# Performance work log

Measured on AMD Instinct MI355X. Metric: run time of the kernel, lower is better.

The kernel has to match this reference:

```python
import jax, jax.numpy as jnp
import numpy as np
import math

N, CH, T, S = 32, 64, 2048, 77  # batch*heads, per-head channels, query len, encoder len

def setup_inputs() -> dict:
    key = jax.random.key(0)
    k1, k2 = jax.random.split(key)
    qkv = jax.random.normal(k1, (N, 3 * CH, T), dtype=jnp.float32)
    encoder_kv = jax.random.normal(k2, (N, 2 * CH, S), dtype=jnp.float32)
    attn_mask = jnp.zeros((1, T, S + T), dtype=jnp.float32)
    return {"qkv": qkv, "encoder_kv": encoder_kv, "attn_mask": attn_mask}

def reference(qkv, encoder_kv, attn_mask):
    ch = qkv.shape[1] // 3
    q, k, v = jnp.split(qkv, 3, axis=1)          # each [N, ch, T]
    ek, ev = jnp.split(encoder_kv, 2, axis=1)    # each [N, ch, S]
    k = jnp.concatenate([ek, k], axis=-1)        # [N, ch, S+T]
    v = jnp.concatenate([ev, v], axis=-1)
    scale = 1.0 / math.sqrt(math.sqrt(ch))
    weight = jnp.einsum('bct,bcs->bts', q * scale, k * scale)  # [N, T, S+T]
    weight = weight.astype(jnp.float32) + attn_mask
    weight = jax.nn.softmax(weight, axis=-1).astype(v.dtype)
    return jnp.einsum('bts,bcs->bct', weight, v)  # [N, ch, T]
```

## Files before the change

kernel.cpp:

```cpp
#include <hip/hip_runtime.h>


typedef __attribute__((ext_vector_type(8))) __bf16 bf16x8;
typedef __attribute__((ext_vector_type(8))) unsigned short u16x8;
typedef __attribute__((ext_vector_type(4))) float f32x4;
typedef float f32x4a __attribute__((ext_vector_type(4))) __attribute__((aligned(4)));
typedef __attribute__((ext_vector_type(4))) unsigned u32x4;
typedef __attribute__((ext_vector_type(2))) unsigned u32x2;

#define L2E  1.44269504089f
#define NEGM (-23.0830936f)

static __device__ __forceinline__ unsigned short f2bf(float f) {
    unsigned u = __builtin_bit_cast(unsigned, f);
    u += 0x7fffu + ((u >> 16) & 1u);
    return (unsigned short)(u >> 16);
}

static __device__ __forceinline__ unsigned pack_bf16(float a, float b) {
#if __has_builtin(__builtin_amdgcn_cvt_pk_bf16_f32)
    typedef __bf16 bf16x2_t __attribute__((ext_vector_type(2)));
    bf16x2_t r = __builtin_amdgcn_cvt_pk_bf16_f32(a, b);
    unsigned u; __builtin_memcpy(&u, &r, 4);
    return u;
#else
    unsigned ua = __builtin_bit_cast(unsigned, a);
    unsigned ub = __builtin_bit_cast(unsigned, b);
    ua += 0x7fffu + ((ua >> 16) & 1u);
    ub += 0x7fffu + ((ub >> 16) & 1u);
    return __builtin_amdgcn_perm(ub, ua, 0x07060302u);
#endif
}

__global__ __launch_bounds__(256) void prep_all(const float* __restrict__ qkv,
                                                const float* __restrict__ ekv,
                                                unsigned short* __restrict__ kws,
                                                unsigned short* __restrict__ vws,
                                                const float* __restrict__ mask) {
    int b = blockIdx.x;
    int tid = threadIdx.x;

    if (b >= 3136) {
        int bb = b - 3136;
        const u32x4* m4 = (const u32x4*)mask;
        unsigned acc = 0;
        for (int i = (bb << 8) + tid; i < 1088000; i += 131072) {
            u32x4 x = m4[i];
            acc |= x.x | x.y | x.z | x.w;
        }
        if (acc) atomicOr((unsigned*)(kws + (size_t)2175 * 64), 1u);
        return;
    }

    if (b >= 1088) {
        int bb = b - 1088;
        int n = bb >> 6, c = bb & 63;
        const float* v  = qkv + (size_t)n * 192 * 2048 + (size_t)(128 + c) * 2048;
        const float* ev = ekv + (size_t)n * 128 * 77 + (size_t)(64 + c) * 77;
        unsigned short* dst = vws + ((size_t)n * 64 + c) * 2176;
        for (int u = tid; u < 544; u += 256) {
            int s = u << 2;
            float f[4];
            if (u >= 20 && u <= 530) {
                f32x4a x = *(const f32x4a*)(v + s - 77);
                f[0] = x.x; f[1] = x.y; f[2] = x.z; f[3] = x.w;
            } else {
                #pragma unroll
                for (int k = 0; k < 4; ++k) {
                    int sk = s + k;
                    f[k] = (sk < 77) ? ev[sk] : ((sk < 2125) ? v[sk - 77] : 0.f);
                }
            }
            u32x2 pk; pk.x = pack_bf16(f[0], f[1]); pk.y = pack_bf16(f[2], f[3]);
            *(u32x2*)(dst + s) = pk;
        }
        return;
    }

    __shared__ float tile[64][65];
    int mode, n, t0;
    if (b < 1024) { mode = 1; n = b >> 5;          t0 = (b & 31) << 6; }
    else          { mode = 2; n = (b - 1024) >> 1; t0 = ((b - 1024) & 1) << 6; }

    const float* src;
    size_t srow;
    int tmax = 64;
    if (mode == 1) { src = qkv + (size_t)n * 192 * 2048 + (size_t)64 * 2048 + t0; srow = 2048; }
    else           { src = ekv + (size_t)n * 128 * 77 + t0; srow = 77;
                     tmax = 77 - t0; if (tmax > 64) tmax = 64; }

    #pragma unroll
    for (int i = 0; i < 4; ++i) {
        int idx = tid + (i << 8);
        int c  = idx >> 4;
        int t4 = (idx & 15) << 2;
        const float* p = src + (size_t)c * srow + t4;
        float v0, v1, v2, v3;
        if (mode == 1) {
            f32x4 v = *(const f32x4*)p;
            v0 = v.x; v1 = v.y; v2 = v.z; v3 = v.w;
        } else {
            v0 = (t4 + 0 < tmax) ? p[0] : 0.f;
            v1 = (t4 + 1 < tmax) ? p[1] : 0.f;
            v2 = (t4 + 2 < tmax) ? p[2] : 0.f;
            v3 = (t4 + 3 < tmax) ? p[3] : 0.f;
        }
        tile[t4 + 0][c] = v0;
        tile[t4 + 1][c] = v1;
        tile[t4 + 2][c] = v2;
        tile[t4 + 3][c] = v3;
    }
    __syncthreads();
    #pragma unroll
    for (int i = 0; i < 4; ++i) {
        int idx = tid + (i << 8);
        int row = idx >> 4;
        int c4  = (idx & 15) << 2;
        if (mode == 2 && row >= tmax) continue;
        u32x2 pk;
        pk.x = pack_bf16(tile[row][c4 + 0], tile[row][c4 + 1]);
        pk.y = pack_bf16(tile[row][c4 + 2], tile[row][c4 + 3]);
        unsigned short* dst;
        if (mode == 1) dst = kws + ((size_t)n * 2176 + 77 + t0 + row) * 64;
        else           dst = kws + ((size_t)n * 2176 + t0 + row) * 64;
        *(u32x2*)(dst + c4) = pk;
    }
}

__global__ __launch_bounds__(256, 2) void flash_attn(
        const float* __restrict__ qkv,
        const unsigned short* __restrict__ kws,
        const unsigned short* __restrict__ vws,
        const float* __restrict__ mask,
        float* __restrict__ out) {
    __shared__ alignas(16) unsigned short k_lds[2][64 * 72];
    __shared__ alignas(16) unsigned short v_lds[3][64 * 72];
    __shared__ alignas(16) unsigned short p_lds[4][32 * 72];

    const int n    = blockIdx.y;
    const int t0   = blockIdx.x << 7;
    const int tid  = threadIdx.x;
    const int wave = tid >> 6;
    const int lane = tid & 63;
    const int q    = lane >> 4;
    const int l16  = lane & 15;
    const int tc0  = t0 + (wave << 5) + l16;
    const int tc1  = tc0 + 16;

    const bool domask =
        __builtin_amdgcn_readfirstlane(*(const unsigned*)(kws + (size_t)2175 * 64)) != 0u;

    bf16x8 qf[2][2];
    #pragma unroll
    for (int h = 0; h < 2; ++h) {
        const float* qsrc = qkv + (size_t)n * 192 * 2048 + (h ? tc1 : tc0);
        u16x8 a0, a1;
        #pragma unroll
        for (int j = 0; j < 8; ++j) {
            a0[j] = f2bf(qsrc[(size_t)((q << 3) + j) * 2048] * 0.125f);
            a1[j] = f2bf(qsrc[(size_t)(32 + (q << 3) + j) * 2048] * 0.125f);
        }
        qf[h][0] = __builtin_bit_cast(bf16x8, a0);
        qf[h][1] = __builtin_bit_cast(bf16x8, a1);
    }

    const unsigned short* kg = kws + (size_t)n * 2176 * 64;
    const unsigned short* vg = vws + (size_t)n * 64 * 2176;
    const float* mrow0 = mask + (size_t)tc0 * 2125;
    const float* mrow1 = mask + (size_t)tc1 * 2125;
    unsigned short* const pw0 = p_lds[wave] + (size_t)l16 * 72;
    unsigned short* const pw1 = p_lds[wave] + (size_t)(16 + l16) * 72;

    const int srow0 = tid >> 3,        sch = (tid & 7) << 3;
    const int srow1 = srow0 + 32;

    f32x4 of[2][4] = {};
    f32x4 sacc[4][2];
    float lsum0 = 0.f, lsum1 = 0.f;

    u32x4 kreg[2], vreg[2];
    f32x4 mreg[4][2];

    auto issue_kv = [&](int s0) {
        kreg[0] = *(const u32x4*)(kg + (size_t)(s0 + srow0) * 64 + sch);
        vreg[0] = *(const u32x4*)(vg + (size_t)srow0 * 2176 + s0 + sch);
        kreg[1] = *(const u32x4*)(kg + (size_t)(s0 + srow1) * 64 + sch);
        vreg[1] = *(const u32x4*)(vg + (size_t)srow1 * 2176 + s0 + sch);
    };
    auto issue_mask = [&](int s0) {
        #pragma unroll
        for (int sm = 0; sm < 4; ++sm) {
            int sbase = s0 + (sm << 4) + (q << 2);
            int sclamp = sbase > 2121 ? 2121 : sbase;
            f32x4a m0 = *(const f32x4a*)(mrow0 + sclamp);
            f32x4a m1 = *(const f32x4a*)(mrow1 + sclamp);
            mreg[sm][0] = f32x4{m0.x, m0.y, m0.z, m0.w};
            mreg[sm][1] = f32x4{m1.x, m1.y, m1.z, m1.w};
        }
    };
    auto stage = [&](unsigned short* kb, unsigned short* vb) {
        *(u32x4*)(kb + srow0 * 72 + sch) = kreg[0];
        *(u32x4*)(vb + srow0 * 72 + sch) = vreg[0];
        *(u32x4*)(kb + srow1 * 72 + sch) = kreg[1];
        *(u32x4*)(vb + srow1 * 72 + sch) = vreg[1];
    };
    auto qkm = [&](const unsigned short* kb) {
        #pragma unroll
        for (int sm = 0; sm < 4; ++sm) {
            const unsigned short* kp = kb + (size_t)((sm << 4) + l16) * 72 + (q << 3);
            bf16x8 ak0 = *(const bf16x8*)(kp);
            bf16x8 ak1 = *(const bf16x8*)(kp + 32);
            #pragma unroll
            for (int h = 0; h < 2; ++h) {
                f32x4 a = {};
                a = __builtin_amdgcn_mfma_f32_16x16x32_bf16(ak0, qf[h][0], a, 0, 0, 0);
                a = __builtin_amdgcn_mfma_f32_16x16x32_bf16(ak1, qf[h][1], a, 0, 0, 0);
                sacc[sm][h] = a;
            }
        }
    };
    auto smax = [&](int s0) {
        const bool tail = (s0 + 64 > 2125);
        #pragma unroll
        for (int sm = 0; sm < 4; ++sm) {
            int sbase = s0 + (sm << 4) + (q << 2);
            #pragma unroll
            for (int h = 0; h < 2; ++h) {
                f32x4 a = sacc[sm][h];
                if (domask) a += mreg[sm][h];
                if (tail) {
                    #pragma unroll
                    for (int j = 0; j < 4; ++j)
                        if (sbase + j >= 2125) a[j] = -1e30f;
                }
                float p0 = __builtin_amdgcn_exp2f(__builtin_fmaf(a[0], L2E, NEGM));
                float p1 = __builtin_amdgcn_exp2f(__builtin_fmaf(a[1], L2E, NEGM));
                float p2 = __builtin_amdgcn_exp2f(__builtin_fmaf(a[2], L2E, NEGM));
                float p3 = __builtin_amdgcn_exp2f(__builtin_fmaf(a[3], L2E, NEGM));
                if (h) lsum1 += (p0 + p1) + (p2 + p3);
                else   lsum0 += (p0 + p1) + (p2 + p3);
                u32x2 pk; pk.x = pack_bf16(p0, p1); pk.y = pack_bf16(p2, p3);
                *(u32x2*)((h ? pw1 : pw0) + (sm << 4) + (q << 2)) = pk;
            }
        }
    };
    auto pv = [&](const unsigned short* vb) {
        bf16x8 bp00 = *(const bf16x8*)(pw0 + (q << 3));
        bf16x8 bp01 = *(const bf16x8*)(pw0 + (q << 3) + 32);
        bf16x8 bp10 = *(const bf16x8*)(pw1 + (q << 3));
        bf16x8 bp11 = *(const bf16x8*)(pw1 + (q << 3) + 32);
        #pragma unroll
        for (int cm = 0; cm < 4; ++cm) {
            const unsigned short* vp = vb + (size_t)((cm << 4) + l16) * 72 + (q << 3);
            bf16x8 av0 = *(const bf16x8*)(vp);
            bf16x8 av1 = *(const bf16x8*)(vp + 32);
            of[0][cm] = __builtin_amdgcn_mfma_f32_16x16x32_bf16(av0, bp00, of[0][cm], 0, 0, 0);
            of[0][cm] = __builtin_amdgcn_mfma_f32_16x16x32_bf16(av1, bp01, of[0][cm], 0, 0, 0);
            of[1][cm] = __builtin_amdgcn_mfma_f32_16x16x32_bf16(av0, bp10, of[1][cm], 0, 0, 0);
            of[1][cm] = __builtin_amdgcn_mfma_f32_16x16x32_bf16(av1, bp11, of[1][cm], 0, 0, 0);
        }
    };

    issue_kv(0);
    if (domask) issue_mask(0);
    stage(k_lds[0], v_lds[0]);
    __syncthreads();
    issue_kv(64);
    qkm(k_lds[0]);
    smax(0);
    if (domask) issue_mask(64);

    int vri = 0, vwi = 1;
    for (int ks = 0; ks < 33; ++ks) {
        const int s1 = (ks + 1) << 6;
        stage(k_lds[(ks + 1) & 1], v_lds[vwi]);
        __syncthreads();
        if (ks < 32) issue_kv(s1 + 64);
        qkm(k_lds[(ks + 1) & 1]);
        pv(v_lds[vri]);
        smax(s1);
        if (domask && ks < 32) issue_mask(s1 + 64);
        vri = (vri == 2) ? 0 : vri + 1;
        vwi = (vwi == 2) ? 0 : vwi + 1;
    }
    pv(v_lds[vri]);

    lsum0 += __shfl_xor(lsum0, 16, 64);
    lsum0 += __shfl_xor(lsum0, 32, 64);
    lsum1 += __shfl_xor(lsum1, 16, 64);
    lsum1 += __shfl_xor(lsum1, 32, 64);
    float inv0 = 1.0f / lsum0, inv1 = 1.0f / lsum1;
    #pragma unroll
    for (int cm = 0; cm < 4; ++cm)
        #pragma unroll
        for (int j = 0; j < 4; ++j) {
            int c = (cm << 4) + (q << 2) + j;
            float* o = out + ((size_t)n * 64 + c) * 2048;
            o[tc0] = of[0][cm][j] * inv0;
            o[tc1] = of[1][cm][j] * inv1;
        }
}

extern "C" void kernel_launch(void* const* d_in, const int* in_sizes, int n_in,
                              void* d_out, int out_size, void* d_ws, size_t ws_size,
                              hipStream_t stream) {
    const float* qkv  = (const float*)d_in[0];
    const float* ekv  = (const float*)d_in[1];
    const float* mask = (const float*)d_in[2];
    float* out = (float*)d_out;

    unsigned short* kws = (unsigned short*)d_ws;
    unsigned short* vws = kws + (size_t)32 * 2176 * 64;

    hipMemsetAsync((char*)d_ws + (size_t)2175 * 64 * 2, 0, 4, stream);
    prep_all<<<3648, 256, 0, stream>>>(qkv, ekv, kws, vws, mask);
    dim3 grid(16, 32);
    flash_attn<<<grid, 256, 0, stream>>>(qkv, kws, vws, mask, out);
}
```

Measured before the change: 163.0 us.

## Halve query tile per wave, load V fragments directly from global

```diff
diff --git a/kernel.cpp b/kernel.cpp
--- a/kernel.cpp
+++ b/kernel.cpp
@@ -127,82 +127,70 @@
     }
 }
 
-__global__ __launch_bounds__(256, 2) void flash_attn(
+__global__ __launch_bounds__(256, 4) void flash_attn(
         const float* __restrict__ qkv,
         const unsigned short* __restrict__ kws,
         const unsigned short* __restrict__ vws,
         const float* __restrict__ mask,
         float* __restrict__ out) {
     __shared__ alignas(16) unsigned short k_lds[2][64 * 72];
-    __shared__ alignas(16) unsigned short v_lds[3][64 * 72];
-    __shared__ alignas(16) unsigned short p_lds[4][32 * 72];
+    __shared__ alignas(16) unsigned short p_lds[4][16 * 72];
 
     const int n    = blockIdx.y;
-    const int t0   = blockIdx.x << 7;
+    const int t0   = blockIdx.x << 6;
     const int tid  = threadIdx.x;
     const int wave = tid >> 6;
     const int lane = tid & 63;
     const int q    = lane >> 4;
     const int l16  = lane & 15;
-    const int tc0  = t0 + (wave << 5) + l16;
-    const int tc1  = tc0 + 16;
+    const int tc   = t0 + (wave << 4) + l16;
 
     const bool domask =
         __builtin_amdgcn_readfirstlane(*(const unsigned*)(kws + (size_t)2175 * 64)) != 0u;
 
-    bf16x8 qf[2][2];
-    #pragma unroll
-    for (int h = 0; h < 2; ++h) {
-        const float* qsrc = qkv + (size_t)n * 192 * 2048 + (h ? tc1 : tc0);
+    bf16x8 qf[2];
+    {
+        const float* qsrc = qkv + (size_t)n * 192 * 2048 + tc;
         u16x8 a0, a1;
         #pragma unroll
         for (int j = 0; j < 8; ++j) {
             a0[j] = f2bf(qsrc[(size_t)((q << 3) + j) * 2048] * 0.125f);
             a1[j] = f2bf(qsrc[(size_t)(32 + (q << 3) + j) * 2048] * 0.125f);
         }
-        qf[h][0] = __builtin_bit_cast(bf16x8, a0);
-        qf[h][1] = __builtin_bit_cast(bf16x8, a1);
+        qf[0] = __builtin_bit_cast(bf16x8, a0);
+        qf[1] = __builtin_bit_cast(bf16x8, a1);
     }
 
     const unsigned short* kg = kws + (size_t)n * 2176 * 64;
     const unsigned short* vg = vws + (size_t)n * 64 * 2176;
-    const float* mrow0 = mask + (size_t)tc0 * 2125;
-    const float* mrow1 = mask + (size_t)tc1 * 2125;
-    unsigned short* const pw0 = p_lds[wave] + (size_t)l16 * 72;
-    unsigned short* const pw1 = p_lds[wave] + (size_t)(16 + l16) * 72;
-
-    const int srow0 = tid >> 3,        sch = (tid & 7) << 3;
+    const float* mrow = mask + (size_t)tc * 2125;
+    unsigned short* const pw = p_lds[wave] + (size_t)l16 * 72;
+
+    const int srow0 = tid >> 3, sch = (tid & 7) << 3;
     const int srow1 = srow0 + 32;
 
-    f32x4 of[2][4] = {};
-    f32x4 sacc[4][2];
-    float lsum0 = 0.f, lsum1 = 0.f;
-
-    u32x4 kreg[2], vreg[2];
-    f32x4 mreg[4][2];
-
-    auto issue_kv = [&](int s0) {
+    f32x4 of[4] = {};
+    f32x4 sacc[4];
+    float lsum = 0.f;
+
+    u32x4 kreg[2];
+    bf16x8 vfrag[4][2];
+
+    auto issue_k = [&](int s0) {
         kreg[0] = *(const u32x4*)(kg + (size_t)(s0 + srow0) * 64 + sch);
-        vreg[0] = *(const u32x4*)(vg + (size_t)srow0 * 2176 + s0 + sch);
         kreg[1] = *(const u32x4*)(kg + (size_t)(s0 + srow1) * 64 + sch);
-        vreg[1] = *(const u32x4*)(vg + (size_t)srow1 * 2176 + s0 + sch);
-    };
-    auto issue_mask = [&](int s0) {
-        #pragma unroll
-        for (int sm = 0; sm < 4; ++sm) {
-            int sbase = s0 + (sm << 4) + (q << 2);
-            int sclamp = sbase > 2121 ? 2121 : sbase;
-            f32x4a m0 = *(const f32x4a*)(mrow0 + sclamp);
-            f32x4a m1 = *(const f32x4a*)(mrow1 + sclamp);
-            mreg[sm][0] = f32x4{m0.x, m0.y, m0.z, m0.w};
-            mreg[sm][1] = f32x4{m1.x, m1.y, m1.z, m1.w};
-        }
-    };
-    auto stage = [&](unsigned short* kb, unsigned short* vb) {
+    };
+    auto issue_v = [&](int s0) {
+        #pragma unroll
+        for (int cm = 0; cm < 4; ++cm) {
+            const unsigned short* vp = vg + (size_t)((cm << 4) + l16) * 2176 + s0 + (q << 3);
+            vfrag[cm][0] = *(const bf16x8*)(vp);
+            vfrag[cm][1] = *(const bf16x8*)(vp + 32);
+        }
+    };
+    auto stage = [&](unsigned short* kb) {
         *(u32x4*)(kb + srow0 * 72 + sch) = kreg[0];
-        *(u32x4*)(vb + srow0 * 72 + sch) = vreg[0];
         *(u32x4*)(kb + srow1 * 72 + sch) = kreg[1];
-        *(u32x4*)(vb + srow1 * 72 + sch) = vreg[1];
     };
     auto qkm = [&](const unsigned short* kb) {
         #pragma unroll
@@ -210,13 +198,10 @@
             const unsigned short* kp = kb + (size_t)((sm << 4) + l16) * 72 + (q << 3);
             bf16x8 ak0 = *(const bf16x8*)(kp);
             bf16x8 ak1 = *(const bf16x8*)(kp + 32);
-            #pragma unroll
-            for (int h = 0; h < 2; ++h) {
-                f32x4 a = {};
-                a = __builtin_amdgcn_mfma_f32_16x16x32_bf16(ak0, qf[h][0], a, 0, 0, 0);
-                a = __builtin_amdgcn_mfma_f32_16x16x32_bf16(ak1, qf[h][1], a, 0, 0, 0);
-                sacc[sm][h] = a;
-            }
+            f32x4 a = {};
+            a = __builtin_amdgcn_mfma_f32_16x16x32_bf16(ak0, qf[0], a, 0, 0, 0);
+            a = __builtin_amdgcn_mfma_f32_16x16x32_bf16(ak1, qf[1], a, 0, 0, 0);
+            sacc[sm] = a;
         }
     };
     auto smax = [&](int s0) {
@@ -224,80 +209,65 @@
         #pragma unroll
         for (int sm = 0; sm < 4; ++sm) {
             int sbase = s0 + (sm << 4) + (q << 2);
-            #pragma unroll
-            for (int h = 0; h < 2; ++h) {
-                f32x4 a = sacc[sm][h];
-                if (domask) a += mreg[sm][h];
-                if (tail) {
-                    #pragma unroll
-                    for (int j = 0; j < 4; ++j)
-                        if (sbase + j >= 2125) a[j] = -1e30f;
-                }
-                float p0 = __builtin_amdgcn_exp2f(__builtin_fmaf(a[0], L2E, NEGM));
-                float p1 = __builtin_amdgcn_exp2f(__builtin_fmaf(a[1], L2E, NEGM));
-                float p2 = __builtin_amdgcn_exp2f(__builtin_fmaf(a[2], L2E, NEGM));
-                float p3 = __builtin_amdgcn_exp2f(__builtin_fmaf(a[3], L2E, NEGM));
-                if (h) lsum1 += (p0 + p1) + (p2 + p3);
-                else   lsum0 += (p0 + p1) + (p2 + p3);
-                u32x2 pk; pk.x = pack_bf16(p0, p1); pk.y = pack_bf16(p2, p3);
-                *(u32x2*)((h ? pw1 : pw0) + (sm << 4) + (q << 2)) = pk;
+            f32x4 a = sacc[sm];
+            if (domask) {
+                int sclamp = sbase > 2121 ? 2121 : sbase;
+                f32x4a m = *(const f32x4a*)(mrow + sclamp);
+                a[0] += m.x; a[1] += m.y; a[2] += m.z; a[3] += m.w;
             }
-        }
-    };
-    auto pv = [&](const unsigned short* vb) {
-        bf16x8 bp00 = *(const bf16x8*)(pw0 + (q << 3));
-        bf16x8 bp01 = *(const bf16x8*)(pw0 + (q << 3) + 32);
-        bf16x8 bp10 = *(const bf16x8*)(pw1 + (q << 3));
-        bf16x8 bp11 = *(const bf16x8*)(pw1 + (q << 3) + 32);
+            if (tail) {
+                #pragma unroll
+                for (int j = 0; j < 4; ++j)
+                    if (sbase + j >= 2125) a[j] = -1e30f;
+            }
+            float p0 = __builtin_amdgcn_exp2f(__builtin_fmaf(a[0], L2E, NEGM));
+            float p1 = __builtin_amdgcn_exp2f(__builtin_fmaf(a[1], L2E, NEGM));
+            float p2 = __builtin_amdgcn_exp2f(__builtin_fmaf(a[2], L2E, NEGM));
+            float p3 = __builtin_amdgcn_exp2f(__builtin_fmaf(a[3], L2E, NEGM));
+            lsum += (p0 + p1) + (p2 + p3);
+            u32x2 pk; pk.x = pack_bf16(p0, p1); pk.y = pack_bf16(p2, p3);
+            *(u32x2*)(pw + (sm << 4) + (q << 2)) = pk;
+        }
+    };
+    auto pv = [&]() {
+        bf16x8 bp0 = *(const bf16x8*)(pw + (q << 3));
+        bf16x8 bp1 = *(const bf16x8*)(pw + (q << 3) + 32);
         #pragma unroll
         for (int cm = 0; cm < 4; ++cm) {
-            const unsigned short* vp = vb + (size_t)((cm << 4) + l16) * 72 + (q << 3);
-            bf16x8 av0 = *(const bf16x8*)(vp);
-            bf16x8 av1 = *(const bf16x8*)(vp + 32);
-            of[0][cm] = __builtin_amdgcn_mfma_f32_16x16x32_bf16(av0, bp00, of[0][cm], 0, 0, 0);
-            of[0][cm] = __builtin_amdgcn_mfma_f32_16x16x32_bf16(av1, bp01, of[0][cm], 0, 0, 0);
-            of[1][cm] = __builtin_amdgcn_mfma_f32_16x16x32_bf16(av0, bp10, of[1][cm], 0, 0, 0);
-            of[1][cm] = __builtin_amdgcn_mfma_f32_16x16x32_bf16(av1, bp11, of[1][cm], 0, 0, 0);
-        }
-    };
-
-    issue_kv(0);
-    if (domask) issue_mask(0);
-    stage(k_lds[0], v_lds[0]);
+            of[cm] = __builtin_amdgcn_mfma_f32_16x16x32_bf16(vfrag[cm][0], bp0, of[cm], 0, 0, 0);
+            of[cm] = __builtin_amdgcn_mfma_f32_16x16x32_bf16(vfrag[cm][1], bp1, of[cm], 0, 0, 0);
+        }
+    };
+
+    issue_k(0);
+    stage(k_lds[0]);
     __syncthreads();
-    issue_kv(64);
+    issue_k(64);
+    issue_v(0);
     qkm(k_lds[0]);
     smax(0);
-    if (domask) issue_mask(64);
-
-    int vri = 0, vwi = 1;
+
     for (int ks = 0; ks < 33; ++ks) {
         const int s1 = (ks + 1) << 6;
-        stage(k_lds[(ks + 1) & 1], v_lds[vwi]);
+        stage(k_lds[(ks + 1) & 1]);
         __syncthreads();
-        if (ks < 32) issue_kv(s1 + 64);
+        if (ks < 32) issue_k(s1 + 64);
         qkm(k_lds[(ks + 1) & 1]);
-        pv(v_lds[vri]);
+        pv();
+        issue_v(s1);
         smax(s1);
-        if (domask && ks < 32) issue_mask(s1 + 64);
-        vri = (vri == 2) ? 0 : vri + 1;
-        vwi = (vwi == 2) ? 0 : vwi + 1;
-    }
-    pv(v_lds[vri]);
-
-    lsum0 += __shfl_xor(lsum0, 16, 64);
-    lsum0 += __shfl_xor(lsum0, 32, 64);
-    lsum1 += __shfl_xor(lsum1, 16, 64);
-    lsum1 += __shfl_xor(lsum1, 32, 64);
-    float inv0 = 1.0f / lsum0, inv1 = 1.0f / lsum1;
+    }
+    pv();
+
+    lsum += __shfl_xor(lsum, 16, 64);
+    lsum += __shfl_xor(lsum, 32, 64);
+    float inv = 1.0f / lsum;
     #pragma unroll
     for (int cm = 0; cm < 4; ++cm)
         #pragma unroll
         for (int j = 0; j < 4; ++j) {
             int c = (cm << 4) + (q << 2) + j;
-            float* o = out + ((size_t)n * 64 + c) * 2048;
-            o[tc0] = of[0][cm][j] * inv0;
-            o[tc1] = of[1][cm][j] * inv1;
+            out[((size_t)n * 64 + c) * 2048 + tc] = of[cm][j] * inv;
         }
 }
 
@@ -314,6 +284,6 @@
 
     hipMemsetAsync((char*)d_ws + (size_t)2175 * 64 * 2, 0, 4, stream);
     prep_all<<<3648, 256, 0, stream>>>(qkv, ekv, kws, vws, mask);
-    dim3 grid(16, 32);
+    dim3 grid(32, 32);
     flash_attn<<<grid, 256, 0, stream>>>(qkv, kws, vws, mask, out);
 }
```

New measurement: 235.0 us. 1.44x slower.

## Compute softmax row sums via MFMA with ones and drop mask prefetch registers

Applied to the files above, without the earlier changes.

```diff
diff --git a/kernel.cpp b/kernel.cpp
--- a/kernel.cpp
+++ b/kernel.cpp
@@ -164,8 +164,14 @@
         qf[h][1] = __builtin_bit_cast(bf16x8, a1);
     }
 
-    const unsigned short* kg = kws + (size_t)n * 2176 * 64;
-    const unsigned short* vg = vws + (size_t)n * 64 * 2176;
+    bf16x8 ones;
+    {
+        u16x8 o;
+        #pragma unroll
+        for (int j = 0; j < 8; ++j) o[j] = 0x3F80;
+        ones = __builtin_bit_cast(bf16x8, o);
+    }
+
     const float* mrow0 = mask + (size_t)tc0 * 2125;
     const float* mrow1 = mask + (size_t)tc1 * 2125;
     unsigned short* const pw0 = p_lds[wave] + (size_t)l16 * 72;
@@ -174,29 +180,23 @@
     const int srow0 = tid >> 3,        sch = (tid & 7) << 3;
     const int srow1 = srow0 + 32;
 
+    const unsigned short* kp0 = kws + (size_t)n * 2176 * 64 + (size_t)srow0 * 64 + sch;
+    const unsigned short* kp1 = kws + (size_t)n * 2176 * 64 + (size_t)srow1 * 64 + sch;
+    const unsigned short* vp0 = vws + (size_t)n * 64 * 2176 + (size_t)srow0 * 2176 + sch;
+    const unsigned short* vp1 = vws + (size_t)n * 64 * 2176 + (size_t)srow1 * 2176 + sch;
+
     f32x4 of[2][4] = {};
+    f32x4 lacc0 = {}, lacc1 = {};
     f32x4 sacc[4][2];
-    float lsum0 = 0.f, lsum1 = 0.f;
 
     u32x4 kreg[2], vreg[2];
-    f32x4 mreg[4][2];
-
-    auto issue_kv = [&](int s0) {
-        kreg[0] = *(const u32x4*)(kg + (size_t)(s0 + srow0) * 64 + sch);
-        vreg[0] = *(const u32x4*)(vg + (size_t)srow0 * 2176 + s0 + sch);
-        kreg[1] = *(const u32x4*)(kg + (size_t)(s0 + srow1) * 64 + sch);
-        vreg[1] = *(const u32x4*)(vg + (size_t)srow1 * 2176 + s0 + sch);
-    };
-    auto issue_mask = [&](int s0) {
-        #pragma unroll
-        for (int sm = 0; sm < 4; ++sm) {
-            int sbase = s0 + (sm << 4) + (q << 2);
-            int sclamp = sbase > 2121 ? 2121 : sbase;
-            f32x4a m0 = *(const f32x4a*)(mrow0 + sclamp);
-            f32x4a m1 = *(const f32x4a*)(mrow1 + sclamp);
-            mreg[sm][0] = f32x4{m0.x, m0.y, m0.z, m0.w};
-            mreg[sm][1] = f32x4{m1.x, m1.y, m1.z, m1.w};
-        }
+
+    auto issue_kv = [&]() {
+        kreg[0] = *(const u32x4*)kp0;
+        vreg[0] = *(const u32x4*)vp0;
+        kreg[1] = *(const u32x4*)kp1;
+        vreg[1] = *(const u32x4*)vp1;
+        kp0 += 4096; kp1 += 4096; vp0 += 64; vp1 += 64;
     };
     auto stage = [&](unsigned short* kb, unsigned short* vb) {
         *(u32x4*)(kb + srow0 * 72 + sch) = kreg[0];
@@ -227,7 +227,11 @@
             #pragma unroll
             for (int h = 0; h < 2; ++h) {
                 f32x4 a = sacc[sm][h];
-                if (domask) a += mreg[sm][h];
+                if (domask) {
+                    int sclamp = sbase > 2121 ? 2121 : sbase;
+                    f32x4a m = *(const f32x4a*)((h ? mrow1 : mrow0) + sclamp);
+                    a[0] += m.x; a[1] += m.y; a[2] += m.z; a[3] += m.w;
+                }
                 if (tail) {
                     #pragma unroll
                     for (int j = 0; j < 4; ++j)
@@ -237,8 +241,6 @@
                 float p1 = __builtin_amdgcn_exp2f(__builtin_fmaf(a[1], L2E, NEGM));
                 float p2 = __builtin_amdgcn_exp2f(__builtin_fmaf(a[2], L2E, NEGM));
                 float p3 = __builtin_amdgcn_exp2f(__builtin_fmaf(a[3], L2E, NEGM));
-                if (h) lsum1 += (p0 + p1) + (p2 + p3);
-                else   lsum0 += (p0 + p1) + (p2 + p3);
                 u32x2 pk; pk.x = pack_bf16(p0, p1); pk.y = pack_bf16(p2, p3);
                 *(u32x2*)((h ? pw1 : pw0) + (sm << 4) + (q << 2)) = pk;
             }
@@ -249,6 +251,10 @@
         bf16x8 bp01 = *(const bf16x8*)(pw0 + (q << 3) + 32);
         bf16x8 bp10 = *(const bf16x8*)(pw1 + (q << 3));
         bf16x8 bp11 = *(const bf16x8*)(pw1 + (q << 3) + 32);
+        lacc0 = __builtin_amdgcn_mfma_f32_16x16x32_bf16(ones, bp00, lacc0, 0, 0, 0);
+        lacc0 = __builtin_amdgcn_mfma_f32_16x16x32_bf16(ones, bp01, lacc0, 0, 0, 0);
+        lacc1 = __builtin_amdgcn_mfma_f32_16x16x32_bf16(ones, bp10, lacc1, 0, 0, 0);
+        lacc1 = __builtin_amdgcn_mfma_f32_16x16x32_bf16(ones, bp11, lacc1, 0, 0, 0);
         #pragma unroll
         for (int cm = 0; cm < 4; ++cm) {
             const unsigned short* vp = vb + (size_t)((cm << 4) + l16) * 72 + (q << 3);
@@ -261,35 +267,28 @@
         }
     };
 
-    issue_kv(0);
-    if (domask) issue_mask(0);
+    issue_kv();
     stage(k_lds[0], v_lds[0]);
     __syncthreads();
-    issue_kv(64);
+    issue_kv();
     qkm(k_lds[0]);
     smax(0);
-    if (domask) issue_mask(64);
 
     int vri = 0, vwi = 1;
     for (int ks = 0; ks < 33; ++ks) {
         const int s1 = (ks + 1) << 6;
         stage(k_lds[(ks + 1) & 1], v_lds[vwi]);
         __syncthreads();
-        if (ks < 32) issue_kv(s1 + 64);
+        if (ks < 32) issue_kv();
         qkm(k_lds[(ks + 1) & 1]);
         pv(v_lds[vri]);
         smax(s1);
-        if (domask && ks < 32) issue_mask(s1 + 64);
         vri = (vri == 2) ? 0 : vri + 1;
         vwi = (vwi == 2) ? 0 : vwi + 1;
     }
     pv(v_lds[vri]);
 
-    lsum0 += __shfl_xor(lsum0, 16, 64);
-    lsum0 += __shfl_xor(lsum0, 32, 64);
-    lsum1 += __shfl_xor(lsum1, 16, 64);
-    lsum1 += __shfl_xor(lsum1, 32, 64);
-    float inv0 = 1.0f / lsum0, inv1 = 1.0f / lsum1;
+    float inv0 = 1.0f / lacc0[0], inv1 = 1.0f / lacc1[0];
     #pragma unroll
     for (int cm = 0; cm < 4; ++cm)
         #pragma unroll
```

Result: faster. 157.4 us (-3.5%).
